# Kernel tuning notes

Hardware: AMD Instinct MI355X
Metric: run time of the kernel (lower is better)

The kernel has to match this reference:

```python
import jax, jax.numpy as jnp
import numpy as np

TOTAL_WORDS = 10000
EMBED = 100
SEQ = 80
UNITS = 64
BATCH = 4096


def setup_inputs() -> dict:
    key = jax.random.key(0)
    ks = jax.random.split(key, 8)
    tokens = jax.random.randint(ks[0], (BATCH, SEQ), 0, TOTAL_WORDS)
    emb = jax.random.normal(ks[1], (TOTAL_WORDS, EMBED), jnp.float32) * 0.05
    W1 = jax.random.normal(ks[2], (EMBED, UNITS), jnp.float32) * (1.0 / np.sqrt(EMBED))
    U1 = jax.random.normal(ks[3], (UNITS, UNITS), jnp.float32) * (1.0 / np.sqrt(UNITS))
    b1 = jnp.zeros((UNITS,), jnp.float32)
    W2 = jax.random.normal(ks[4], (UNITS, UNITS), jnp.float32) * (1.0 / np.sqrt(UNITS))
    U2 = jax.random.normal(ks[5], (UNITS, UNITS), jnp.float32) * (1.0 / np.sqrt(UNITS))
    b2 = jnp.zeros((UNITS,), jnp.float32)
    Wo = jax.random.normal(ks[6], (UNITS, 1), jnp.float32) * (1.0 / np.sqrt(UNITS))
    bo = jnp.zeros((1,), jnp.float32)
    return {"tokens": tokens, "emb": emb, "W1": W1, "U1": U1, "b1": b1,
            "W2": W2, "U2": U2, "b2": b2, "Wo": Wo, "bo": bo}


def reference(tokens, emb, W1, U1, b1, W2, U2, b2, Wo, bo):
    # Embedding lookup: [B, T, E]
    x = emb[tokens]
    # Precompute input projections for layer 1 across all timesteps: [B, T, U]
    xw1 = jnp.einsum('bte,eu->btu', x, W1) + b1
    B = tokens.shape[0]
    h0 = jnp.zeros((B, UNITS), xw1.dtype)

    def step(carry, inp):
        h1, h2 = carry
        h1 = jnp.tanh(inp + h1 @ U1)                 # SimpleRNN layer 1
        h2 = jnp.tanh(h1 @ W2 + b2 + h2 @ U2)        # SimpleRNN layer 2 consumes layer-1 seq
        return (h1, h2), None

    (_, h2), _ = jax.lax.scan(step, (h0, h0), jnp.swapaxes(xw1, 0, 1))
    # Dense(1) head + sigmoid: [B, 1]
    return jax.nn.sigmoid(h2 @ Wo + bo)
```

## Files before the change

kernel.cpp:

```cpp
#include <hip/hip_runtime.h>

#define BATCH 4096
#define SEQ   80
#define EMBED 100
#define UNITS 64
#define NTILE (BATCH / 16)
#define NVOC  10000
#define NVWV  ((NVOC + 15) / 16)
#define NPAIR2 (SEQ / 2)

typedef float f32x4  __attribute__((ext_vector_type(4)));
typedef short bf16x8 __attribute__((ext_vector_type(8)));

#define MFMA16 __builtin_amdgcn_mfma_f32_16x16x32_bf16

#define TAB_OFF 0u
#define XW2_OFF 1280000u

__device__ __forceinline__ unsigned f2bfu(float f) {
    union { float f; unsigned u; } x; x.f = f;
    return (x.u + 0x7fffu + ((x.u >> 16) & 1u)) >> 16;
}
__device__ __forceinline__ unsigned cvtpk(float lo, float hi) {
    unsigned r;
    asm("v_cvt_pk_bf16_f32 %0, %1, %2" : "=v"(r) : "v"(lo), "v"(hi));
    return r;
}
__device__ __forceinline__ float bflo(unsigned u) {
    union { unsigned u; float f; } x; x.u = u << 16; return x.f;
}
__device__ __forceinline__ float bfhi(unsigned u) {
    union { unsigned u; float f; } x; x.u = u & 0xffff0000u; return x.f;
}
__device__ __forceinline__ float fast_tanh(float x) {
    float e = __builtin_amdgcn_exp2f(x * 2.8853900817779268f);
    float r = __builtin_amdgcn_rcpf(e + 1.0f);
    return __builtin_fmaf(-2.0f, r, 1.0f);
}

__global__ __launch_bounds__(256) void tableproj_kernel(
    const float* __restrict__ emb,
    const float* __restrict__ b1,
    const float* __restrict__ W1,
    char* __restrict__ table)
{
    const int lane = threadIdx.x & 63;
    const int wid  = threadIdx.x >> 6;
    const int gw   = blockIdx.x * 4 + wid;
    if (gw >= NVWV) return;
    const int m15  = lane & 15;
    const int kgrp = lane >> 4;
    const int v    = gw * 16 + m15;
    const int vc   = v < NVOC ? v : NVOC - 1;

    bf16x8 aW1[4][4];
    #pragma unroll
    for (int mt = 0; mt < 4; ++mt) {
        const int u = 16 * mt + m15;
        #pragma unroll
        for (int ks = 0; ks < 4; ++ks)
            #pragma unroll
            for (int j = 0; j < 8; ++j) {
                const int k = kgrp * 8 + j + 32 * ks;
                aW1[mt][ks][j] = (k < EMBED) ? (short)f2bfu(W1[k * UNITS + u])
                                             : (short)0;
            }
    }

    const float* rp = emb + (size_t)vc * EMBED;
    bf16x8 bf[4];
    #pragma unroll
    for (int ks = 0; ks < 3; ++ks) {
        f32x4 e0 = *(const f32x4*)(rp + kgrp * 8 + 32 * ks);
        f32x4 e1 = *(const f32x4*)(rp + kgrp * 8 + 32 * ks + 4);
        uint4 u;
        u.x = cvtpk(e0.x, e0.y); u.y = cvtpk(e0.z, e0.w);
        u.z = cvtpk(e1.x, e1.y); u.w = cvtpk(e1.z, e1.w);
        bf[ks] = *(bf16x8*)&u;
    }
    {
        uint4 u = {0u, 0u, 0u, 0u};
        if (kgrp == 0) {
            f32x4 e0 = *(const f32x4*)(rp + 96);
            u.x = cvtpk(e0.x, e0.y); u.y = cvtpk(e0.z, e0.w);
        }
        bf[3] = *(bf16x8*)&u;
    }

    f32x4 acc[4];
    #pragma unroll
    for (int mt = 0; mt < 4; ++mt)
        acc[mt] = *(const f32x4*)(b1 + 16 * mt + 4 * kgrp);
    #pragma unroll
    for (int ks = 0; ks < 4; ++ks)
        #pragma unroll
        for (int mt = 0; mt < 4; ++mt)
            acc[mt] = MFMA16(aW1[mt][ks], bf[ks], acc[mt], 0, 0, 0);

    #pragma unroll
    for (int mt = 0; mt < 4; ++mt) {
        uint2 q;
        q.x = cvtpk(acc[mt][0], acc[mt][1]);
        q.y = cvtpk(acc[mt][2], acc[mt][3]);
        *(uint2*)(table + (size_t)v * 128 + mt * 32 + kgrp * 8) = q;
    }
}

__global__ __launch_bounds__(256, 1) void rnn_kernel(
    const int*    __restrict__ tokens,
    const uint2*  __restrict__ table,
    uint4*        __restrict__ xw2,
    const float*  __restrict__ U1,
    const float*  __restrict__ W2,
    const float*  __restrict__ U2,
    const float*  __restrict__ b2,
    const float*  __restrict__ Wo,
    const float*  __restrict__ bo,
    float*        __restrict__ out)
{
    __shared__ __align__(16) char h1L[2][2048];
    __shared__ __align__(16) char h2L[2][2048];
    __shared__ int   tokL[16][84];
    __shared__ float headp[4][16];

    const int lane = threadIdx.x & 63;
    const int w    = threadIdx.x >> 6;
    const int m15  = lane & 15;
    const int kgrp = lane >> 4;
    const int swz  = (m15 & 7) << 4;
    const int wg   = blockIdx.x;

    {
        uint4 z = {0u, 0u, 0u, 0u};
        if (threadIdx.x < 128) ((uint4*)h2L[0])[threadIdx.x] = z;
    }
    for (int i = threadIdx.x; i < 16 * SEQ; i += 256) {
        const int r = i / SEQ;
        const int t = i - r * SEQ;
        tokL[r][t] = tokens[(size_t)(wg * 16 + r) * SEQ + t];
    }

    const int urow = 16 * w + m15;
    bf16x8 aU1[2], aW2[2], aU2[2];
    #pragma unroll
    for (int ks = 0; ks < 2; ++ks)
        #pragma unroll
        for (int j = 0; j < 8; ++j) {
            const int k = kgrp * 8 + j + 32 * ks;
            aU1[ks][j] = (short)f2bfu(U1[k * UNITS + urow]);
            aW2[ks][j] = (short)f2bfu(W2[k * UNITS + urow]);
            aU2[ks][j] = (short)f2bfu(U2[k * UNITS + urow]);
        }
    const int ubase = 16 * w + 4 * kgrp;
    const f32x4 b2c = *(const f32x4*)(b2 + ubase);

    __syncthreads();

    const uint2* tabp = table + w * 4 + kgrp;
    uint4* outp = xw2 + ((size_t)(wg * 4 + w)) * NPAIR2 * 64 + lane;
    uint4 r0, r1, r2;
    #pragma unroll 8
    for (int pk = 0; pk < NPAIR2; ++pk) {
        const int tokE = tokL[m15][2 * pk];
        const int tokO = tokL[m15][2 * pk + 1];
        uint2 gE = tabp[(size_t)tokE * 16];
        uint2 gO = tabp[(size_t)tokO * 16];
        uint4 o; o.x = gE.x; o.y = gE.y; o.z = gO.x; o.w = gO.y;
        if (pk == 0)      r0 = o;
        else if (pk == 1) r1 = o;
        else if (pk == 2) r2 = o;
        else              outp[(size_t)pk * 64] = o;
    }
    asm volatile("s_waitcnt vmcnt(0)" ::: "memory");

    {
        float t0 = fast_tanh(bflo(r0.x)), t1 = fast_tanh(bfhi(r0.x));
        float t2 = fast_tanh(bflo(r0.y)), t3 = fast_tanh(bfhi(r0.y));
        uint2 pk; pk.x = cvtpk(t0, t1); pk.y = cvtpk(t2, t3);
        *(uint2*)(h1L[0] + m15 * 128 + ((32 * w + 8 * kgrp) ^ swz)) = pk;
    }
    asm volatile("s_waitcnt lgkmcnt(0)" ::: "memory");
    __builtin_amdgcn_s_barrier();

    float d2f0 = 0.f, d2f1 = 0.f, d2f2 = 0.f, d2f3 = 0.f;

#define LBAR() do { asm volatile("s_waitcnt lgkmcnt(0)" ::: "memory"); \
                    __builtin_amdgcn_s_barrier(); } while (0)
#define PHASE(QX, QY, P, Q)                                                      \
  {                                                                              \
    bf16x8 bh1a = *(const bf16x8*)(h1L[P] + m15 * 128 + ((kgrp * 16     ) ^ swz)); \
    bf16x8 bh1b = *(const bf16x8*)(h1L[P] + m15 * 128 + ((kgrp * 16 + 64) ^ swz)); \
    bf16x8 bh2a = *(const bf16x8*)(h2L[P] + m15 * 128 + ((kgrp * 16     ) ^ swz)); \
    bf16x8 bh2b = *(const bf16x8*)(h2L[P] + m15 * 128 + ((kgrp * 16 + 64) ^ swz)); \
    f32x4 d1 = {bflo(QX), bfhi(QX), bflo(QY), bfhi(QY)};                         \
    d1 = MFMA16(aU1[0], bh1a, d1, 0, 0, 0);                                      \
    d1 = MFMA16(aU1[1], bh1b, d1, 0, 0, 0);                                      \
    f32x4 dC = b2c;                                                              \
    dC = MFMA16(aW2[0], bh1a, dC, 0, 0, 0);                                      \
    dC = MFMA16(aW2[1], bh1b, dC, 0, 0, 0);                                      \
    f32x4 dD = {0.f, 0.f, 0.f, 0.f};                                             \
    dD = MFMA16(aU2[0], bh2a, dD, 0, 0, 0);                                      \
    dD = MFMA16(aU2[1], bh2b, dD, 0, 0, 0);                                      \
    float n0 = fast_tanh(d1[0]);                                                 \
    float n1 = fast_tanh(d1[1]);                                                 \
    float n2 = fast_tanh(d1[2]);                                                 \
    float n3 = fast_tanh(d1[3]);                                                 \
    d2f0 = fast_tanh(dC[0] + dD[0]);                                             \
    d2f1 = fast_tanh(dC[1] + dD[1]);                                             \
    d2f2 = fast_tanh(dC[2] + dD[2]);                                             \
    d2f3 = fast_tanh(dC[3] + dD[3]);                                             \
    {                                                                            \
        uint2 pk; pk.x = cvtpk(n0, n1); pk.y = cvtpk(n2, n3);                    \
        *(uint2*)(h1L[Q] + m15 * 128 + ((32 * w + 8 * kgrp) ^ swz)) = pk;        \
    }                                                                            \
    {                                                                            \
        uint2 pk; pk.x = cvtpk(d2f0, d2f1); pk.y = cvtpk(d2f2, d2f3);            \
        *(uint2*)(h2L[Q] + m15 * 128 + ((32 * w + 8 * kgrp) ^ swz)) = pk;        \
    }                                                                            \
    LBAR();                                                                      \
  }

    const uint4* xwp = (const uint4*)outp;
    for (int k = 0; k < NPAIR2; ++k) {
        const int pn = (k + 3 < NPAIR2) ? k + 3 : NPAIR2 - 1;
        uint4 r3 = xwp[(size_t)pn * 64];
        PHASE(r0.z, r0.w, 0, 1)
        PHASE(r1.x, r1.y, 1, 0)
        r0 = r1; r1 = r2; r2 = r3;
    }
#undef PHASE
#undef LBAR

    const f32x4 woc = *(const f32x4*)(Wo + ubase);
    float p = d2f0 * woc[0] + d2f1 * woc[1] + d2f2 * woc[2] + d2f3 * woc[3];
    p += __shfl_xor(p, 16, 64);
    p += __shfl_xor(p, 32, 64);
    if (lane < 16) headp[w][lane] = p;
    __syncthreads();
    if (threadIdx.x < 16) {
        const float z = headp[0][threadIdx.x] + headp[1][threadIdx.x]
                      + headp[2][threadIdx.x] + headp[3][threadIdx.x] + bo[0];
        const float e = __builtin_amdgcn_exp2f(-z * 1.4426950408889634f);
        out[wg * 16 + threadIdx.x] = __builtin_amdgcn_rcpf(1.0f + e);
    }
}

extern "C" void kernel_launch(void* const* d_in, const int* in_sizes, int n_in,
                              void* d_out, int out_size, void* d_ws, size_t ws_size,
                              hipStream_t stream) {
    const int*   tokens = (const int*)  d_in[0];
    const float* emb    = (const float*)d_in[1];
    const float* W1     = (const float*)d_in[2];
    const float* U1     = (const float*)d_in[3];
    const float* b1     = (const float*)d_in[4];
    const float* W2     = (const float*)d_in[5];
    const float* U2     = (const float*)d_in[6];
    const float* b2     = (const float*)d_in[7];
    const float* Wo     = (const float*)d_in[8];
    const float* bo     = (const float*)d_in[9];
    float* out = (float*)d_out;
    char*  ws  = (char*)d_ws;

    tableproj_kernel<<<(NVWV + 3) / 4, 256, 0, stream>>>(
        emb, b1, W1, ws + TAB_OFF);
    rnn_kernel<<<NTILE, 256, 0, stream>>>(
        tokens, (const uint2*)(ws + TAB_OFF), (uint4*)(ws + XW2_OFF),
        U1, W2, U2, b2, Wo, bo, out);
}
```

Baseline: 55.64 us.

## Keep gathered per-timestep input projections in registers instead of workspace round-trip

Instead of gathering the table rows for all timesteps, writing them to a global workspace buffer and re-reading them three steps ahead during the recurrence, each thread now gathers all 80 timestep values into a register array up front. The recurrence loop is fully unrolled so the array stays in registers. This removes the global store and reload traffic and the prefetch logic. In exchange it uses 160 extra VGPRs per thread, with spill risk, and a larger unrolled code body; launch bounds allow one block per CU.

```diff
diff --git a/kernel.cpp b/kernel.cpp
--- a/kernel.cpp
+++ b/kernel.cpp
@@ -15,7 +15,6 @@
 #define MFMA16 __builtin_amdgcn_mfma_f32_16x16x32_bf16
 
 #define TAB_OFF 0u
-#define XW2_OFF 1280000u
 
 __device__ __forceinline__ unsigned f2bfu(float f) {
     union { float f; unsigned u; } x; x.f = f;
@@ -109,7 +108,6 @@
 __global__ __launch_bounds__(256, 1) void rnn_kernel(
     const int*    __restrict__ tokens,
     const uint2*  __restrict__ table,
-    uint4*        __restrict__ xw2,
     const float*  __restrict__ U1,
     const float*  __restrict__ W2,
     const float*  __restrict__ U2,
@@ -157,25 +155,14 @@
     __syncthreads();
 
     const uint2* tabp = table + w * 4 + kgrp;
-    uint4* outp = xw2 + ((size_t)(wg * 4 + w)) * NPAIR2 * 64 + lane;
-    uint4 r0, r1, r2;
-    #pragma unroll 8
-    for (int pk = 0; pk < NPAIR2; ++pk) {
-        const int tokE = tokL[m15][2 * pk];
-        const int tokO = tokL[m15][2 * pk + 1];
-        uint2 gE = tabp[(size_t)tokE * 16];
-        uint2 gO = tabp[(size_t)tokO * 16];
-        uint4 o; o.x = gE.x; o.y = gE.y; o.z = gO.x; o.w = gO.y;
-        if (pk == 0)      r0 = o;
-        else if (pk == 1) r1 = o;
-        else if (pk == 2) r2 = o;
-        else              outp[(size_t)pk * 64] = o;
-    }
-    asm volatile("s_waitcnt vmcnt(0)" ::: "memory");
+    uint2 xr[SEQ];
+    #pragma unroll
+    for (int t = 0; t < SEQ; ++t)
+        xr[t] = tabp[(size_t)tokL[m15][t] * 16];
 
     {
-        float t0 = fast_tanh(bflo(r0.x)), t1 = fast_tanh(bfhi(r0.x));
-        float t2 = fast_tanh(bflo(r0.y)), t3 = fast_tanh(bfhi(r0.y));
+        float t0 = fast_tanh(bflo(xr[0].x)), t1 = fast_tanh(bfhi(xr[0].x));
+        float t2 = fast_tanh(bflo(xr[0].y)), t3 = fast_tanh(bfhi(xr[0].y));
         uint2 pk; pk.x = cvtpk(t0, t1); pk.y = cvtpk(t2, t3);
         *(uint2*)(h1L[0] + m15 * 128 + ((32 * w + 8 * kgrp) ^ swz)) = pk;
     }
@@ -186,13 +173,13 @@
 
 #define LBAR() do { asm volatile("s_waitcnt lgkmcnt(0)" ::: "memory"); \
                     __builtin_amdgcn_s_barrier(); } while (0)
-#define PHASE(QX, QY, P, Q)                                                      \
+#define PHASE(Q2, P, Q)                                                          \
   {                                                                              \
     bf16x8 bh1a = *(const bf16x8*)(h1L[P] + m15 * 128 + ((kgrp * 16     ) ^ swz)); \
     bf16x8 bh1b = *(const bf16x8*)(h1L[P] + m15 * 128 + ((kgrp * 16 + 64) ^ swz)); \
     bf16x8 bh2a = *(const bf16x8*)(h2L[P] + m15 * 128 + ((kgrp * 16     ) ^ swz)); \
     bf16x8 bh2b = *(const bf16x8*)(h2L[P] + m15 * 128 + ((kgrp * 16 + 64) ^ swz)); \
-    f32x4 d1 = {bflo(QX), bfhi(QX), bflo(QY), bfhi(QY)};                         \
+    f32x4 d1 = {bflo((Q2).x), bfhi((Q2).x), bflo((Q2).y), bfhi((Q2).y)};         \
     d1 = MFMA16(aU1[0], bh1a, d1, 0, 0, 0);                                      \
     d1 = MFMA16(aU1[1], bh1b, d1, 0, 0, 0);                                      \
     f32x4 dC = b2c;                                                              \
@@ -220,13 +207,10 @@
     LBAR();                                                                      \
   }
 
-    const uint4* xwp = (const uint4*)outp;
+    #pragma unroll
     for (int k = 0; k < NPAIR2; ++k) {
-        const int pn = (k + 3 < NPAIR2) ? k + 3 : NPAIR2 - 1;
-        uint4 r3 = xwp[(size_t)pn * 64];
-        PHASE(r0.z, r0.w, 0, 1)
-        PHASE(r1.x, r1.y, 1, 0)
-        r0 = r1; r1 = r2; r2 = r3;
+        PHASE(xr[2 * k + 1], 0, 1)
+        PHASE(xr[(2 * k + 2 < SEQ) ? 2 * k + 2 : SEQ - 1], 1, 0)
     }
 #undef PHASE
 #undef LBAR
@@ -264,6 +248,6 @@
     tableproj_kernel<<<(NVWV + 3) / 4, 256, 0, stream>>>(
         emb, b1, W1, ws + TAB_OFF);
     rnn_kernel<<<NTILE, 256, 0, stream>>>(
-        tokens, (const uint2*)(ws + TAB_OFF), (uint4*)(ws + XW2_OFF),
+        tokens, (const uint2*)(ws + TAB_OFF),
         U1, W2, U2, b2, Wo, bo, out);
 }
```

New measurement: 45.54 us. 1.22x faster.
